# Optimization experiments

Measured on AMD Instinct MI355X. Metric: run time of the kernel, lower is better.

Reference implementation:

```python
import jax, jax.numpy as jnp
import numpy as np

B, H, W = 4, 256, 256
DIM, DIM_OUT, NUM_HEADS = 96, 192, 3
WS = 8            # window_size
QS = 2            # q_stride (2,2)
HIDDEN = int(DIM_OUT * 4.0)
EPS = 1e-6


def layernorm(x, g, b):
    m = jnp.mean(x, axis=-1, keepdims=True)
    v = jnp.mean(jnp.square(x - m), axis=-1, keepdims=True)
    return (x - m) * jax.lax.rsqrt(v + EPS) * g + b


def maxpool2x2(x):
    # x: [..., h, w, c] -> [..., h//2, w//2, c]
    s = x.shape
    x = x.reshape(s[:-3] + (s[-3] // QS, QS, s[-2] // QS, QS, s[-1]))
    return x.max(axis=(-4, -2))


def setup_inputs() -> dict:
    key = jax.random.key(0)
    ks = jax.random.split(key, 16)
    std = 0.02
    return {
        "x": jax.random.normal(ks[0], (B, H, W, DIM), dtype=jnp.float32),
        "norm1_g": jnp.ones((DIM,), jnp.float32),
        "norm1_b": jnp.zeros((DIM,), jnp.float32),
        "proj_w": jax.random.normal(ks[1], (DIM, DIM_OUT), jnp.float32) * std,
        "proj_b": jnp.zeros((DIM_OUT,), jnp.float32),
        "qkv_w": jax.random.normal(ks[2], (DIM, 3 * DIM_OUT), jnp.float32) * std,
        "qkv_b": jnp.zeros((3 * DIM_OUT,), jnp.float32),
        "attn_proj_w": jax.random.normal(ks[3], (DIM_OUT, DIM_OUT), jnp.float32) * std,
        "attn_proj_b": jnp.zeros((DIM_OUT,), jnp.float32),
        "norm2_g": jnp.ones((DIM_OUT,), jnp.float32),
        "norm2_b": jnp.zeros((DIM_OUT,), jnp.float32),
        "mlp_w1": jax.random.normal(ks[4], (DIM_OUT, HIDDEN), jnp.float32) * std,
        "mlp_b1": jnp.zeros((HIDDEN,), jnp.float32),
        "mlp_w2": jax.random.normal(ks[5], (HIDDEN, DIM_OUT), jnp.float32) * std,
        "mlp_b2": jnpp_zeros if False else jnp.zeros((DIM_OUT,), jnp.float32),
    }


def reference(x, norm1_g, norm1_b, proj_w, proj_b, qkv_w, qkv_b,
              attn_proj_w, attn_proj_b, norm2_g, norm2_b,
              mlp_w1, mlp_b1, mlp_w2, mlp_b2):
    b, h, w, _ = x.shape
    xn = layernorm(x, norm1_g, norm1_b)

    # dim != dim_out: shortcut = proj(norm(x)), then pooled by q_stride
    shortcut = xn @ proj_w + proj_b                       # [B,H,W,Do]
    shortcut = maxpool2x2(shortcut)                       # [B,H/2,W/2,Do]

    # window partition (H,W divisible by WS -> no padding)
    nh, nw = h // WS, w // WS
    xw = xn.reshape(b, nh, WS, nw, WS, DIM).transpose(0, 1, 3, 2, 4, 5)
    xw = xw.reshape(b * nh * nw, WS, WS, DIM)             # [Bw,WS,WS,C]
    Bw = xw.shape[0]

    # MultiScaleAttention with q pooling
    hd = DIM_OUT // NUM_HEADS
    qkv = (xw @ qkv_w + qkv_b).reshape(Bw, WS * WS, 3, NUM_HEADS, hd)
    q, k, v = qkv[:, :, 0], qkv[:, :, 1], qkv[:, :, 2]    # [Bw,N,h,d]
    q = maxpool2x2(q.reshape(Bw, WS, WS, DIM_OUT))        # [Bw,WS/2,WS/2,Do]
    wq = WS // QS
    q = q.reshape(Bw, wq * wq, NUM_HEADS, hd)

    scale = 1.0 / jnp.sqrt(jnp.asarray(hd, x.dtype))
    scores = jnp.einsum('bqhd,bkhd->bhqk', q, k) * scale
    probs = jax.nn.softmax(scores, axis=-1)
    out = jnp.einsum('bhqk,bkhd->bqhd', probs, v).reshape(Bw, wq, wq, DIM_OUT)
    out = out @ attn_proj_w + attn_proj_b                 # [Bw,wq,wq,Do]

    # window unpartition at pooled resolution
    hp, wp = h // QS, w // QS
    out = out.reshape(b, nh, nw, wq, wq, DIM_OUT).transpose(0, 1, 3, 2, 4, 5)
    out = out.reshape(b, hp, wp, DIM_OUT)

    y = shortcut + out
    yn = layernorm(y, norm2_g, norm2_b)
    mlp = jax.nn.gelu(yn @ mlp_w1 + mlp_b1, approximate=False) @ mlp_w2 + mlp_b2
    return y + mlp
```

## Files before the change

### kernel.cpp

```cpp
#include <hip/hip_runtime.h>
#include <hip/hip_bf16.h>
#include <math.h>

#define EPSV 1e-6f

typedef __attribute__((ext_vector_type(8))) short bf16x8;
typedef __attribute__((ext_vector_type(4))) float f32x4;
typedef __attribute__((ext_vector_type(4))) unsigned short u16x4;

__device__ inline float bf2f(unsigned short u) {
  union { unsigned int i; float f; } v;
  v.i = ((unsigned int)u) << 16;
  return v.f;
}
__device__ inline unsigned short f2bf(float f) {
  unsigned int u = __builtin_bit_cast(unsigned int, f);
  u += 0x7FFFu + ((u >> 16) & 1u);
  return (unsigned short)(u >> 16);
}
__device__ inline float fast_gelu(float v) {
  float u = 1.5957691216057308f * (v + 0.044715f * v * v * v);
  float t = __expf(-u);
  return v * __builtin_amdgcn_rcpf(1.f + t);
}

__global__ __launch_bounds__(256) void k0_pack(
    const float* __restrict__ qw, const float* __restrict__ aw,
    const float* __restrict__ w1, const float* __restrict__ w2,
    const float* __restrict__ pw, unsigned short* __restrict__ qwp,
    unsigned short* __restrict__ awp, unsigned short* __restrict__ w1p,
    unsigned short* __restrict__ w2p, unsigned short* __restrict__ pwp) {
  int idx = blockIdx.x * 256 + threadIdx.x;
  int lane = idx & 63;
  int l15 = lane & 15, quad = lane >> 4;
  if (idx < 6912) {
    int fi = idx >> 6;
    int ntile = fi / 3, kstep = fi - ntile * 3;
    int n = ntile * 16 + l15, k0 = kstep * 32 + quad * 8;
#pragma unroll
    for (int j = 0; j < 8; ++j)
      qwp[(size_t)idx * 8 + j] = f2bf(qw[(size_t)(k0 + j) * 576 + n]);
  } else if (idx < 11520) {
    int i2 = idx - 6912;
    int fi = i2 >> 6;
    int ntile = fi / 6, kstep = fi - ntile * 6;
    int n = ntile * 16 + l15, k0 = kstep * 32 + quad * 8;
#pragma unroll
    for (int j = 0; j < 8; ++j)
      awp[(size_t)i2 * 8 + j] = f2bf(aw[(size_t)(k0 + j) * 192 + n]);
  } else if (idx < 29952) {
    int i3 = idx - 11520;
    int fi = i3 >> 6;
    int ntile = fi / 6, kstep = fi - ntile * 6;
    int n = ntile * 16 + l15, k0 = kstep * 32 + quad * 8;
#pragma unroll
    for (int j = 0; j < 8; ++j)
      w1p[(size_t)i3 * 8 + j] = f2bf(w1[(size_t)(k0 + j) * 768 + n]);
  } else if (idx < 48384) {
    int i4 = idx - 29952;
    int fi = i4 >> 6;
    int ntile = fi / 24, kstep = fi - ntile * 24;
    int n = ntile * 16 + l15, k0 = kstep * 32 + quad * 8;
#pragma unroll
    for (int j = 0; j < 8; ++j)
      w2p[(size_t)i4 * 8 + j] = f2bf(w2[(size_t)(k0 + j) * 192 + n]);
  } else if (idx < 50688) {
    int i5 = idx - 48384;
    int fi = i5 >> 6;
    int ntile = fi / 3, kstep = fi - ntile * 3;
    int n = ntile * 16 + l15, k0 = kstep * 32 + quad * 8;
#pragma unroll
    for (int j = 0; j < 8; ++j)
      pwp[(size_t)i5 * 8 + j] = f2bf(pw[(size_t)(k0 + j) * 192 + n]);
  }
}

__global__ __launch_bounds__(256) void k123_fused(
    const float* __restrict__ x, const float* __restrict__ n1g,
    const float* __restrict__ n1b, const unsigned short* __restrict__ pwp,
    const float* __restrict__ pb, const unsigned short* __restrict__ qwp,
    const float* __restrict__ qb, const unsigned short* __restrict__ awp,
    const float* __restrict__ ab, float* __restrict__ out) {
  __shared__ unsigned short kk[64][200];
  __shared__ unsigned short vT[192][72];
  __shared__ unsigned short wbuf[3][16][72];
  __shared__ union {
    unsigned short xn[64][104];
    float sc[16][200];
  } u;

  int tid = threadIdx.x, wave = tid >> 6, lane = tid & 63;
  int wi = blockIdx.x;
  int b = wi >> 10, nh = (wi >> 5) & 31, nw = wi & 31;
  int grow0 = nh * 8, gcol0 = nw * 8;
  int l15 = lane & 15, quad = lane >> 4;

  {
    int tt = tid >> 2, sub = tid & 3;
    int rr = tt >> 3, cc = tt & 7;
    size_t tok = (size_t)((b * 256 + grow0 + rr) * 256 + gcol0 + cc);
    const f32x4* xr4 = (const f32x4*)(x + tok * 96 + sub * 24);
    f32x4 v[6];
#pragma unroll
    for (int i = 0; i < 6; ++i) v[i] = xr4[i];
    float s = 0.f;
#pragma unroll
    for (int i = 0; i < 6; ++i)
#pragma unroll
      for (int j = 0; j < 4; ++j) s += v[i][j];
    s += __shfl_xor(s, 1);
    s += __shfl_xor(s, 2);
    float mean = s * (1.f / 96.f);
    float q = 0.f;
#pragma unroll
    for (int i = 0; i < 6; ++i)
#pragma unroll
      for (int j = 0; j < 4; ++j) {
        float d = v[i][j] - mean;
        q += d * d;
      }
    q += __shfl_xor(q, 1);
    q += __shfl_xor(q, 2);
    float rstd = rsqrtf(q * (1.f / 96.f) + EPSV);
    const f32x4* g4 = (const f32x4*)(n1g + sub * 24);
    const f32x4* b4 = (const f32x4*)(n1b + sub * 24);
#pragma unroll
    for (int i = 0; i < 6; ++i) {
      f32x4 gg = g4[i], bb = b4[i];
      u16x4 o;
#pragma unroll
      for (int j = 0; j < 4; ++j)
        o[j] = f2bf((v[i][j] - mean) * rstd * gg[j] + bb[j]);
      *(u16x4*)(&u.xn[tt][sub * 24 + i * 4]) = o;
    }
  }
  __syncthreads();

  bf16x8 areg[4][3];
#pragma unroll
  for (int mt = 0; mt < 4; ++mt)
#pragma unroll
    for (int ks = 0; ks < 3; ++ks)
      areg[mt][ks] = *(const bf16x8*)(&u.xn[mt * 16 + l15][ks * 32 + quad * 8]);
  __syncthreads();

#pragma unroll
  for (int nl = 0; nl < 3; ++nl) {
    int nt = wave * 3 + nl;
    const unsigned short* bp = pwp + ((size_t)(nt * 3) * 64 + lane) * 8;
    bf16x8 b0 = *(const bf16x8*)(bp);
    bf16x8 b1 = *(const bf16x8*)(bp + 512);
    bf16x8 b2 = *(const bf16x8*)(bp + 1024);
    int c = nt * 16 + l15;
    float bias = pb[c];
#pragma unroll
    for (int mt = 0; mt < 4; ++mt) {
      f32x4 acc = {0.f, 0.f, 0.f, 0.f};
      acc = __builtin_amdgcn_mfma_f32_16x16x32_bf16(areg[mt][0], b0, acc, 0, 0, 0);
      acc = __builtin_amdgcn_mfma_f32_16x16x32_bf16(areg[mt][1], b1, acc, 0, 0, 0);
      acc = __builtin_amdgcn_mfma_f32_16x16x32_bf16(areg[mt][2], b2, acc, 0, 0, 0);
      float p0 = fmaxf(acc[0], acc[1]);
      float p1 = fmaxf(acc[2], acc[3]);
      float q0 = fmaxf(p0, __shfl_xor(p0, 32));
      float q1 = fmaxf(p1, __shfl_xor(p1, 32));
      if (quad < 2) {
        int p = mt * 4 + quad * 2;
        u.sc[p][c] = q0 + bias;
        u.sc[p + 1][c] = q1 + bias;
      }
    }
  }

#pragma unroll
  for (int aj = 0; aj < 9; ++aj) {
    int type, hh, nt;
    if (wave < 3) {
      if (aj < 4) { type = 0; hh = wave; nt = aj; }
      else { int kv = wave * 5 + (aj - 4); type = 1 + kv / 12; int t2 = kv % 12; hh = t2 >> 2; nt = t2 & 3; }
    } else {
      int kv = 15 + aj; type = 1 + kv / 12; int t2 = kv % 12; hh = t2 >> 2; nt = t2 & 3;
    }
    int gnt = type * 12 + hh * 4 + nt;
    const unsigned short* bp = qwp + (size_t)gnt * 1536 + lane * 8;
    bf16x8 b0 = *(const bf16x8*)(bp);
    bf16x8 b1 = *(const bf16x8*)(bp + 512);
    bf16x8 b2 = *(const bf16x8*)(bp + 1024);
    int dloc = nt * 16 + l15;
    int dglob = hh * 64 + dloc;
    float bias = qb[type * 192 + dglob];
#pragma unroll
    for (int mt = 0; mt < 4; ++mt) {
      f32x4 acc = {0.f, 0.f, 0.f, 0.f};
      acc = __builtin_amdgcn_mfma_f32_16x16x32_bf16(areg[mt][0], b0, acc, 0, 0, 0);
      acc = __builtin_amdgcn_mfma_f32_16x16x32_bf16(areg[mt][1], b1, acc, 0, 0, 0);
      acc = __builtin_amdgcn_mfma_f32_16x16x32_bf16(areg[mt][2], b2, acc, 0, 0, 0);
      if (type == 0) {
        float p0 = fmaxf(acc[0], acc[1]);
        float p1 = fmaxf(acc[2], acc[3]);
        float q0 = fmaxf(p0, __shfl_xor(p0, 32));
        float q1 = fmaxf(p1, __shfl_xor(p1, 32));
        if (quad < 2) {
          int p = mt * 4 + quad * 2;
          wbuf[wave][p][dloc] = f2bf(q0 + bias);
          wbuf[wave][p + 1][dloc] = f2bf(q1 + bias);
        }
      } else if (type == 1) {
        int t0 = mt * 16 + quad * 4;
#pragma unroll
        for (int r = 0; r < 4; ++r) kk[t0 + r][dglob] = f2bf(acc[r] + bias);
      } else {
        int t0 = mt * 16 + quad * 4;
        u16x4 pk;
#pragma unroll
        for (int r = 0; r < 4; ++r) pk[r] = f2bf(acc[r] + bias);
        *(u16x4*)(&vT[dglob][t0]) = pk;
      }
    }
  }
  __syncthreads();

  f32x4 o4[4];
  if (wave < 3) {
    int h = wave;
    bf16x8 aq0 = *(const bf16x8*)(&wbuf[wave][l15][quad * 8]);
    bf16x8 aq1 = *(const bf16x8*)(&wbuf[wave][l15][32 + quad * 8]);
    f32x4 s4[4];
#pragma unroll
    for (int kt = 0; kt < 4; ++kt) {
      bf16x8 bk0 = *(const bf16x8*)(&kk[kt * 16 + l15][h * 64 + quad * 8]);
      bf16x8 bk1 = *(const bf16x8*)(&kk[kt * 16 + l15][h * 64 + 32 + quad * 8]);
      f32x4 s = {0.f, 0.f, 0.f, 0.f};
      s = __builtin_amdgcn_mfma_f32_16x16x32_bf16(aq0, bk0, s, 0, 0, 0);
      s = __builtin_amdgcn_mfma_f32_16x16x32_bf16(aq1, bk1, s, 0, 0, 0);
      s4[kt] = s;
    }
    float ps[4][4];
#pragma unroll
    for (int r = 0; r < 4; ++r) {
      float m = fmaxf(fmaxf(s4[0][r], s4[1][r]), fmaxf(s4[2][r], s4[3][r]));
#pragma unroll
      for (int o = 8; o; o >>= 1) m = fmaxf(m, __shfl_xor(m, o));
      float sm = 0.f;
#pragma unroll
      for (int kt = 0; kt < 4; ++kt) {
        float e = __expf((s4[kt][r] - m) * 0.125f);
        ps[kt][r] = e;
        sm += e;
      }
#pragma unroll
      for (int o = 8; o; o >>= 1) sm += __shfl_xor(sm, o);
      float inv = __builtin_amdgcn_rcpf(sm);
#pragma unroll
      for (int kt = 0; kt < 4; ++kt) ps[kt][r] *= inv;
    }
#pragma unroll
    for (int kt = 0; kt < 4; ++kt)
#pragma unroll
      for (int r = 0; r < 4; ++r)
        wbuf[wave][quad * 4 + r][kt * 16 + l15] = f2bf(ps[kt][r]);
    bf16x8 ap0 = *(const bf16x8*)(&wbuf[wave][l15][quad * 8]);
    bf16x8 ap1 = *(const bf16x8*)(&wbuf[wave][l15][32 + quad * 8]);
#pragma unroll
    for (int dt = 0; dt < 4; ++dt) {
      bf16x8 bv0 = *(const bf16x8*)(&vT[h * 64 + dt * 16 + l15][quad * 8]);
      bf16x8 bv1 = *(const bf16x8*)(&vT[h * 64 + dt * 16 + l15][32 + quad * 8]);
      f32x4 o = {0.f, 0.f, 0.f, 0.f};
      o = __builtin_amdgcn_mfma_f32_16x16x32_bf16(ap0, bv0, o, 0, 0, 0);
      o = __builtin_amdgcn_mfma_f32_16x16x32_bf16(ap1, bv1, o, 0, 0, 0);
      o4[dt] = o;
    }
  }
  __syncthreads();

  if (wave < 3) {
    int h = wave;
#pragma unroll
    for (int dt = 0; dt < 4; ++dt)
#pragma unroll
      for (int r = 0; r < 4; ++r)
        kk[quad * 4 + r][h * 64 + dt * 16 + l15] = f2bf(o4[dt][r]);
  }
  __syncthreads();

  bf16x8 ao[6];
#pragma unroll
  for (int ks = 0; ks < 6; ++ks)
    ao[ks] = *(const bf16x8*)(&kk[l15][ks * 32 + quad * 8]);
#pragma unroll
  for (int nl = 0; nl < 3; ++nl) {
    int ntl = wave * 3 + nl;
    const unsigned short* bp = awp + (size_t)ntl * 3072 + lane * 8;
    f32x4 acc = {0.f, 0.f, 0.f, 0.f};
#pragma unroll
    for (int ks = 0; ks < 6; ++ks) {
      bf16x8 bw = *(const bf16x8*)(bp + ks * 512);
      acc = __builtin_amdgcn_mfma_f32_16x16x32_bf16(ao[ks], bw, acc, 0, 0, 0);
    }
    int cc = ntl * 16 + l15;
    float bias = ab[cc];
#pragma unroll
    for (int r = 0; r < 4; ++r) {
      int p = quad * 4 + r;
      int hp = nh * 4 + (p >> 2), wp2 = nw * 4 + (p & 3);
      size_t oi = ((size_t)((b * 128 + hp) * 128 + wp2)) * 192 + cc;
      out[oi] = u.sc[p][cc] + acc[r] + bias;
    }
  }
}

__global__ __launch_bounds__(256) void k4_mlp(
    float* __restrict__ y, const float* __restrict__ g,
    const float* __restrict__ bt, const unsigned short* __restrict__ w1p,
    const float* __restrict__ b1, const unsigned short* __restrict__ w2p,
    const float* __restrict__ b2) {
  __shared__ unsigned short yn[32][196];
  __shared__ unsigned short hls[32][196];
  int tid = threadIdx.x, wave = tid >> 6, lane = tid & 63;
  int l15 = lane & 15, quad = lane >> 4;
  size_t tokbase = (size_t)blockIdx.x * 32;

  for (int j = 0; j < 8; ++j) {
    int tt = wave * 8 + j;
    const float* yr = y + (tokbase + tt) * 192;
    float v0 = yr[lane], v1 = yr[64 + lane], v2 = yr[128 + lane];
    float s = v0 + v1 + v2;
#pragma unroll
    for (int o = 32; o; o >>= 1) s += __shfl_xor(s, o);
    float mean = s * (1.f / 192.f);
    float d0 = v0 - mean, d1 = v1 - mean, d2 = v2 - mean;
    float q = d0 * d0 + d1 * d1 + d2 * d2;
#pragma unroll
    for (int o = 32; o; o >>= 1) q += __shfl_xor(q, o);
    float rstd = rsqrtf(q * (1.f / 192.f) + EPSV);
    yn[tt][lane] = f2bf(d0 * rstd * g[lane] + bt[lane]);
    yn[tt][64 + lane] = f2bf(d1 * rstd * g[64 + lane] + bt[64 + lane]);
    yn[tt][128 + lane] = f2bf(d2 * rstd * g[128 + lane] + bt[128 + lane]);
  }
  __syncthreads();

  bf16x8 ar[2][6];
#pragma unroll
  for (int mt = 0; mt < 2; ++mt)
#pragma unroll
    for (int ks = 0; ks < 6; ++ks)
      ar[mt][ks] = *(const bf16x8*)(&yn[mt * 16 + l15][ks * 32 + quad * 8]);

  f32x4 acc2[3][2];
#pragma unroll
  for (int nl = 0; nl < 3; ++nl)
#pragma unroll
    for (int mt = 0; mt < 2; ++mt) acc2[nl][mt] = (f32x4){0.f, 0.f, 0.f, 0.f};

  for (int c = 0; c < 4; ++c) {
#pragma unroll
    for (int nl = 0; nl < 3; ++nl) {
      int gnt = c * 12 + wave * 3 + nl;
      const unsigned short* bp = w1p + ((size_t)(gnt * 6) * 64 + lane) * 8;
      f32x4 t0 = {0.f, 0.f, 0.f, 0.f}, t1 = {0.f, 0.f, 0.f, 0.f};
#pragma unroll
      for (int ks = 0; ks < 6; ++ks) {
        bf16x8 bw = *(const bf16x8*)(bp + ks * 512);
        t0 = __builtin_amdgcn_mfma_f32_16x16x32_bf16(ar[0][ks], bw, t0, 0, 0, 0);
        t1 = __builtin_amdgcn_mfma_f32_16x16x32_bf16(ar[1][ks], bw, t1, 0, 0, 0);
      }
      int lcol = wave * 48 + nl * 16 + l15;
      float bias = b1[c * 192 + lcol];
#pragma unroll
      for (int r = 0; r < 4; ++r) {
        hls[quad * 4 + r][lcol] = f2bf(fast_gelu(t0[r] + bias));
        hls[16 + quad * 4 + r][lcol] = f2bf(fast_gelu(t1[r] + bias));
      }
    }
    __syncthreads();
    bf16x8 hr[2][6];
#pragma unroll
    for (int mt = 0; mt < 2; ++mt)
#pragma unroll
      for (int ks = 0; ks < 6; ++ks)
        hr[mt][ks] = *(const bf16x8*)(&hls[mt * 16 + l15][ks * 32 + quad * 8]);
#pragma unroll
    for (int nl = 0; nl < 3; ++nl) {
      int nt2 = wave * 3 + nl;
      const unsigned short* bp =
          w2p + ((size_t)((nt2 * 24 + c * 6)) * 64 + lane) * 8;
#pragma unroll
      for (int ks = 0; ks < 6; ++ks) {
        bf16x8 bw = *(const bf16x8*)(bp + ks * 512);
        acc2[nl][0] =
            __builtin_amdgcn_mfma_f32_16x16x32_bf16(hr[0][ks], bw, acc2[nl][0], 0, 0, 0);
        acc2[nl][1] =
            __builtin_amdgcn_mfma_f32_16x16x32_bf16(hr[1][ks], bw, acc2[nl][1], 0, 0, 0);
      }
    }
    __syncthreads();
  }

#pragma unroll
  for (int nl = 0; nl < 3; ++nl) {
    int col = (wave * 3 + nl) * 16 + l15;
    float bias = b2[col];
#pragma unroll
    for (int mt = 0; mt < 2; ++mt) {
#pragma unroll
      for (int r = 0; r < 4; ++r) {
        size_t oi = (tokbase + mt * 16 + quad * 4 + r) * 192 + col;
        y[oi] += acc2[nl][mt][r] + bias;
      }
    }
  }
}

extern "C" void kernel_launch(void* const* d_in, const int* in_sizes, int n_in,
                              void* d_out, int out_size, void* d_ws,
                              size_t ws_size, hipStream_t stream) {
  const float* x = (const float*)d_in[0];
  const float* n1g = (const float*)d_in[1];
  const float* n1b = (const float*)d_in[2];
  const float* pw = (const float*)d_in[3];
  const float* pb = (const float*)d_in[4];
  const float* qw = (const float*)d_in[5];
  const float* qb = (const float*)d_in[6];
  const float* aw = (const float*)d_in[7];
  const float* ab = (const float*)d_in[8];
  const float* n2g = (const float*)d_in[9];
  const float* n2b = (const float*)d_in[10];
  const float* w1 = (const float*)d_in[11];
  const float* b1 = (const float*)d_in[12];
  const float* w2 = (const float*)d_in[13];
  const float* b2 = (const float*)d_in[14];
  float* out = (float*)d_out;

  char* wsb = (char*)d_ws;
  unsigned short* qwp = (unsigned short*)wsb;
  unsigned short* awp = (unsigned short*)(wsb + 110592);
  unsigned short* w1p = (unsigned short*)(wsb + 184320);
  unsigned short* w2p = (unsigned short*)(wsb + 479232);
  unsigned short* pwp = (unsigned short*)(wsb + 774144);

  hipLaunchKernelGGL(k0_pack, dim3(198), dim3(256), 0, stream, qw, aw, w1, w2,
                     pw, qwp, awp, w1p, w2p, pwp);
  hipLaunchKernelGGL(k123_fused, dim3(4096), dim3(256), 0, stream, x, n1g,
                     n1b, pwp, pb, qwp, qb, awp, ab, out);
  hipLaunchKernelGGL(k4_mlp, dim3(2048), dim3(256), 0, stream, out, n2g, n2b,
                     w1p, b1, w2p, b2);
}
```

Baseline: 359.7 us.

## Fuse LayerNorm2 and MLP into the per-window attention kernel

Merges the separate MLP kernel into the per-window attention kernel. The residual sum y stays in shared memory and goes through LayerNorm2 and the two MLP GEMMs on the window's 16 pooled tokens before a single write to global memory. This removes the global round trip of y (write, read, read-modify-write) and one kernel launch. The cost is that each block now processes only 16 tokens, with M=16 MFMA tiles instead of 32. So MLP weights are reread from L2 per window twice as often, and shared memory use grows to about 73KB, which may reduce occupancy.

```diff
diff --git a/kernel.cpp b/kernel.cpp
--- a/kernel.cpp
+++ b/kernel.cpp
@@ -75,19 +75,23 @@
   }
 }
 
-__global__ __launch_bounds__(256) void k123_fused(
+__global__ __launch_bounds__(256) void k1234_fused(
     const float* __restrict__ x, const float* __restrict__ n1g,
     const float* __restrict__ n1b, const unsigned short* __restrict__ pwp,
     const float* __restrict__ pb, const unsigned short* __restrict__ qwp,
     const float* __restrict__ qb, const unsigned short* __restrict__ awp,
-    const float* __restrict__ ab, float* __restrict__ out) {
-  __shared__ unsigned short kk[64][200];
-  __shared__ unsigned short vT[192][72];
-  __shared__ unsigned short wbuf[3][16][72];
-  __shared__ union {
-    unsigned short xn[64][104];
-    float sc[16][200];
-  } u;
+    const float* __restrict__ ab, const float* __restrict__ n2g,
+    const float* __restrict__ n2b, const unsigned short* __restrict__ w1p,
+    const float* __restrict__ b1, const unsigned short* __restrict__ w2p,
+    const float* __restrict__ b2, float* __restrict__ out) {
+  __shared__ __align__(16) unsigned char smem[72960];
+  unsigned short (*kk)[200] = (unsigned short (*)[200])smem;
+  unsigned short (*vT)[72] = (unsigned short (*)[72])(smem + 25600);
+  unsigned short (*wbuf)[16][72] =
+      (unsigned short (*)[16][72])(smem + 53248);
+  float (*sc)[200] = (float (*)[200])(smem + 60160);
+  unsigned short (*yn)[196] = (unsigned short (*)[196])(smem + 25600);
+  unsigned short (*hls)[196] = (unsigned short (*)[196])(smem + 25600 + 6272);
 
   int tid = threadIdx.x, wave = tid >> 6, lane = tid & 63;
   int wi = blockIdx.x;
@@ -131,7 +135,7 @@
 #pragma unroll
       for (int j = 0; j < 4; ++j)
         o[j] = f2bf((v[i][j] - mean) * rstd * gg[j] + bb[j]);
-      *(u16x4*)(&u.xn[tt][sub * 24 + i * 4]) = o;
+      *(u16x4*)(&kk[tt][sub * 24 + i * 4]) = o;
     }
   }
   __syncthreads();
@@ -141,7 +145,7 @@
   for (int mt = 0; mt < 4; ++mt)
 #pragma unroll
     for (int ks = 0; ks < 3; ++ks)
-      areg[mt][ks] = *(const bf16x8*)(&u.xn[mt * 16 + l15][ks * 32 + quad * 8]);
+      areg[mt][ks] = *(const bf16x8*)(&kk[mt * 16 + l15][ks * 32 + quad * 8]);
   __syncthreads();
 
 #pragma unroll
@@ -149,24 +153,24 @@
     int nt = wave * 3 + nl;
     const unsigned short* bp = pwp + ((size_t)(nt * 3) * 64 + lane) * 8;
     bf16x8 b0 = *(const bf16x8*)(bp);
-    bf16x8 b1 = *(const bf16x8*)(bp + 512);
-    bf16x8 b2 = *(const bf16x8*)(bp + 1024);
+    bf16x8 b1v = *(const bf16x8*)(bp + 512);
+    bf16x8 b2v = *(const bf16x8*)(bp + 1024);
     int c = nt * 16 + l15;
     float bias = pb[c];
 #pragma unroll
     for (int mt = 0; mt < 4; ++mt) {
       f32x4 acc = {0.f, 0.f, 0.f, 0.f};
       acc = __builtin_amdgcn_mfma_f32_16x16x32_bf16(areg[mt][0], b0, acc, 0, 0, 0);
-      acc = __builtin_amdgcn_mfma_f32_16x16x32_bf16(areg[mt][1], b1, acc, 0, 0, 0);
-      acc = __builtin_amdgcn_mfma_f32_16x16x32_bf16(areg[mt][2], b2, acc, 0, 0, 0);
+      acc = __builtin_amdgcn_mfma_f32_16x16x32_bf16(areg[mt][1], b1v, acc, 0, 0, 0);
+      acc = __builtin_amdgcn_mfma_f32_16x16x32_bf16(areg[mt][2], b2v, acc, 0, 0, 0);
       float p0 = fmaxf(acc[0], acc[1]);
       float p1 = fmaxf(acc[2], acc[3]);
       float q0 = fmaxf(p0, __shfl_xor(p0, 32));
       float q1 = fmaxf(p1, __shfl_xor(p1, 32));
       if (quad < 2) {
         int p = mt * 4 + quad * 2;
-        u.sc[p][c] = q0 + bias;
-        u.sc[p + 1][c] = q1 + bias;
+        sc[p][c] = q0 + bias;
+        sc[p + 1][c] = q1 + bias;
       }
     }
   }
@@ -183,8 +187,8 @@
     int gnt = type * 12 + hh * 4 + nt;
     const unsigned short* bp = qwp + (size_t)gnt * 1536 + lane * 8;
     bf16x8 b0 = *(const bf16x8*)(bp);
-    bf16x8 b1 = *(const bf16x8*)(bp + 512);
-    bf16x8 b2 = *(const bf16x8*)(bp + 1024);
+    bf16x8 b1v = *(const bf16x8*)(bp + 512);
+    bf16x8 b2v = *(const bf16x8*)(bp + 1024);
     int dloc = nt * 16 + l15;
     int dglob = hh * 64 + dloc;
     float bias = qb[type * 192 + dglob];
@@ -192,8 +196,8 @@
     for (int mt = 0; mt < 4; ++mt) {
       f32x4 acc = {0.f, 0.f, 0.f, 0.f};
       acc = __builtin_amdgcn_mfma_f32_16x16x32_bf16(areg[mt][0], b0, acc, 0, 0, 0);
-      acc = __builtin_amdgcn_mfma_f32_16x16x32_bf16(areg[mt][1], b1, acc, 0, 0, 0);
-      acc = __builtin_amdgcn_mfma_f32_16x16x32_bf16(areg[mt][2], b2, acc, 0, 0, 0);
+      acc = __builtin_amdgcn_mfma_f32_16x16x32_bf16(areg[mt][1], b1v, acc, 0, 0, 0);
+      acc = __builtin_amdgcn_mfma_f32_16x16x32_bf16(areg[mt][2], b2v, acc, 0, 0, 0);
       if (type == 0) {
         float p0 = fmaxf(acc[0], acc[1]);
         float p1 = fmaxf(acc[2], acc[3]);
@@ -301,95 +305,94 @@
 #pragma unroll
     for (int r = 0; r < 4; ++r) {
       int p = quad * 4 + r;
-      int hp = nh * 4 + (p >> 2), wp2 = nw * 4 + (p & 3);
-      size_t oi = ((size_t)((b * 128 + hp) * 128 + wp2)) * 192 + cc;
-      out[oi] = u.sc[p][cc] + acc[r] + bias;
-    }
-  }
-}
-
-__global__ __launch_bounds__(256) void k4_mlp(
-    float* __restrict__ y, const float* __restrict__ g,
-    const float* __restrict__ bt, const unsigned short* __restrict__ w1p,
-    const float* __restrict__ b1, const unsigned short* __restrict__ w2p,
-    const float* __restrict__ b2) {
-  __shared__ unsigned short yn[32][196];
-  __shared__ unsigned short hls[32][196];
-  int tid = threadIdx.x, wave = tid >> 6, lane = tid & 63;
-  int l15 = lane & 15, quad = lane >> 4;
-  size_t tokbase = (size_t)blockIdx.x * 32;
-
-  for (int j = 0; j < 8; ++j) {
-    int tt = wave * 8 + j;
-    const float* yr = y + (tokbase + tt) * 192;
-    float v0 = yr[lane], v1 = yr[64 + lane], v2 = yr[128 + lane];
-    float s = v0 + v1 + v2;
-#pragma unroll
-    for (int o = 32; o; o >>= 1) s += __shfl_xor(s, o);
+      sc[p][cc] += acc[r] + bias;
+    }
+  }
+  __syncthreads();
+
+  {
+    int tt = wave * 4 + quad;
+    const f32x4* y4 = (const f32x4*)(&sc[tt][l15 * 12]);
+    f32x4 vv[3];
+    vv[0] = y4[0]; vv[1] = y4[1]; vv[2] = y4[2];
+    float s = 0.f;
+#pragma unroll
+    for (int i = 0; i < 3; ++i)
+#pragma unroll
+      for (int j = 0; j < 4; ++j) s += vv[i][j];
+    s += __shfl_xor(s, 1);
+    s += __shfl_xor(s, 2);
+    s += __shfl_xor(s, 4);
+    s += __shfl_xor(s, 8);
     float mean = s * (1.f / 192.f);
-    float d0 = v0 - mean, d1 = v1 - mean, d2 = v2 - mean;
-    float q = d0 * d0 + d1 * d1 + d2 * d2;
-#pragma unroll
-    for (int o = 32; o; o >>= 1) q += __shfl_xor(q, o);
+    float q = 0.f;
+#pragma unroll
+    for (int i = 0; i < 3; ++i)
+#pragma unroll
+      for (int j = 0; j < 4; ++j) {
+        float d = vv[i][j] - mean;
+        q += d * d;
+      }
+    q += __shfl_xor(q, 1);
+    q += __shfl_xor(q, 2);
+    q += __shfl_xor(q, 4);
+    q += __shfl_xor(q, 8);
     float rstd = rsqrtf(q * (1.f / 192.f) + EPSV);
-    yn[tt][lane] = f2bf(d0 * rstd * g[lane] + bt[lane]);
-    yn[tt][64 + lane] = f2bf(d1 * rstd * g[64 + lane] + bt[64 + lane]);
-    yn[tt][128 + lane] = f2bf(d2 * rstd * g[128 + lane] + bt[128 + lane]);
-  }
-  __syncthreads();
-
-  bf16x8 ar[2][6];
-#pragma unroll
-  for (int mt = 0; mt < 2; ++mt)
-#pragma unroll
-    for (int ks = 0; ks < 6; ++ks)
-      ar[mt][ks] = *(const bf16x8*)(&yn[mt * 16 + l15][ks * 32 + quad * 8]);
-
-  f32x4 acc2[3][2];
-#pragma unroll
-  for (int nl = 0; nl < 3; ++nl)
-#pragma unroll
-    for (int mt = 0; mt < 2; ++mt) acc2[nl][mt] = (f32x4){0.f, 0.f, 0.f, 0.f};
+    const f32x4* g4 = (const f32x4*)(n2g + l15 * 12);
+    const f32x4* b4 = (const f32x4*)(n2b + l15 * 12);
+#pragma unroll
+    for (int i = 0; i < 3; ++i) {
+      f32x4 gg = g4[i], bb = b4[i];
+      u16x4 o;
+#pragma unroll
+      for (int j = 0; j < 4; ++j)
+        o[j] = f2bf((vv[i][j] - mean) * rstd * gg[j] + bb[j]);
+      *(u16x4*)(&yn[tt][l15 * 12 + i * 4]) = o;
+    }
+  }
+  __syncthreads();
+
+  bf16x8 ar[6];
+#pragma unroll
+  for (int ks = 0; ks < 6; ++ks)
+    ar[ks] = *(const bf16x8*)(&yn[l15][ks * 32 + quad * 8]);
+
+  f32x4 acc2[3];
+#pragma unroll
+  for (int nl = 0; nl < 3; ++nl) acc2[nl] = (f32x4){0.f, 0.f, 0.f, 0.f};
 
   for (int c = 0; c < 4; ++c) {
 #pragma unroll
     for (int nl = 0; nl < 3; ++nl) {
       int gnt = c * 12 + wave * 3 + nl;
       const unsigned short* bp = w1p + ((size_t)(gnt * 6) * 64 + lane) * 8;
-      f32x4 t0 = {0.f, 0.f, 0.f, 0.f}, t1 = {0.f, 0.f, 0.f, 0.f};
+      f32x4 t0 = {0.f, 0.f, 0.f, 0.f};
 #pragma unroll
       for (int ks = 0; ks < 6; ++ks) {
         bf16x8 bw = *(const bf16x8*)(bp + ks * 512);
-        t0 = __builtin_amdgcn_mfma_f32_16x16x32_bf16(ar[0][ks], bw, t0, 0, 0, 0);
-        t1 = __builtin_amdgcn_mfma_f32_16x16x32_bf16(ar[1][ks], bw, t1, 0, 0, 0);
+        t0 = __builtin_amdgcn_mfma_f32_16x16x32_bf16(ar[ks], bw, t0, 0, 0, 0);
       }
       int lcol = wave * 48 + nl * 16 + l15;
       float bias = b1[c * 192 + lcol];
 #pragma unroll
-      for (int r = 0; r < 4; ++r) {
+      for (int r = 0; r < 4; ++r)
         hls[quad * 4 + r][lcol] = f2bf(fast_gelu(t0[r] + bias));
-        hls[16 + quad * 4 + r][lcol] = f2bf(fast_gelu(t1[r] + bias));
-      }
     }
     __syncthreads();
-    bf16x8 hr[2][6];
-#pragma unroll
-    for (int mt = 0; mt < 2; ++mt)
-#pragma unroll
-      for (int ks = 0; ks < 6; ++ks)
-        hr[mt][ks] = *(const bf16x8*)(&hls[mt * 16 + l15][ks * 32 + quad * 8]);
+    bf16x8 hr[6];
+#pragma unroll
+    for (int ks = 0; ks < 6; ++ks)
+      hr[ks] = *(const bf16x8*)(&hls[l15][ks * 32 + quad * 8]);
 #pragma unroll
     for (int nl = 0; nl < 3; ++nl) {
       int nt2 = wave * 3 + nl;
       const unsigned short* bp =
-          w2p + ((size_t)((nt2 * 24 + c * 6)) * 64 + lane) * 8;
+          w2p + ((size_t)(nt2 * 24 + c * 6) * 64 + lane) * 8;
 #pragma unroll
       for (int ks = 0; ks < 6; ++ks) {
         bf16x8 bw = *(const bf16x8*)(bp + ks * 512);
-        acc2[nl][0] =
-            __builtin_amdgcn_mfma_f32_16x16x32_bf16(hr[0][ks], bw, acc2[nl][0], 0, 0, 0);
-        acc2[nl][1] =
-            __builtin_amdgcn_mfma_f32_16x16x32_bf16(hr[1][ks], bw, acc2[nl][1], 0, 0, 0);
+        acc2[nl] =
+            __builtin_amdgcn_mfma_f32_16x16x32_bf16(hr[ks], bw, acc2[nl], 0, 0, 0);
       }
     }
     __syncthreads();
@@ -400,12 +403,11 @@
     int col = (wave * 3 + nl) * 16 + l15;
     float bias = b2[col];
 #pragma unroll
-    for (int mt = 0; mt < 2; ++mt) {
-#pragma unroll
-      for (int r = 0; r < 4; ++r) {
-        size_t oi = (tokbase + mt * 16 + quad * 4 + r) * 192 + col;
-        y[oi] += acc2[nl][mt][r] + bias;
-      }
+    for (int r = 0; r < 4; ++r) {
+      int p = quad * 4 + r;
+      int hp = nh * 4 + (p >> 2), wp2 = nw * 4 + (p & 3);
+      size_t oi = ((size_t)((b * 128 + hp) * 128 + wp2)) * 192 + col;
+      out[oi] = sc[p][col] + acc2[nl][r] + bias;
     }
   }
 }
@@ -439,8 +441,7 @@
 
   hipLaunchKernelGGL(k0_pack, dim3(198), dim3(256), 0, stream, qw, aw, w1, w2,
                      pw, qwp, awp, w1p, w2p, pwp);
-  hipLaunchKernelGGL(k123_fused, dim3(4096), dim3(256), 0, stream, x, n1g,
-                     n1b, pwp, pb, qwp, qb, awp, ab, out);
-  hipLaunchKernelGGL(k4_mlp, dim3(2048), dim3(256), 0, stream, out, n2g, n2b,
-                     w1p, b1, w2p, b2);
-}
+  hipLaunchKernelGGL(k1234_fused, dim3(4096), dim3(256), 0, stream, x, n1g,
+                     n1b, pwp, pb, qwp, qb, awp, ab, n2g, n2b, w1p, b1, w2p,
+                     b2, out);
+}
```

After: 361.5 us. Within noise of the previous version (+0.5%).
